# Kernel optimization log

Hardware: AMD Instinct MI355X
Metric: run time of the kernel (lower is better)

The kernel has to match this reference:

```python
import jax, jax.numpy as jnp
import numpy as np

VNUMS = [4248, 4258, 5327, 3721, 5404, 2818]
B, C, H, W = 12, 64, 192, 192
DV, HID, BOX = 128, 256, 32


def _roi_patches(imgs, pros, imgbatch, box_len=BOX):
    # torchvision roi_align (aligned=False, sampling_ratio -> 1 sample per 1x1 bin):
    # bilinear sample at bin centers x1 + (j+0.5), y1 + (i+0.5)
    ar = jnp.arange(box_len, dtype=pros.dtype) + 0.5
    xs = pros[:, 0:1] - box_len / 2.0 + ar  # [G, box]
    ys = pros[:, 1:2] - box_len / 2.0 + ar  # [G, box]
    img_g = imgs[imgbatch]  # [G, C, H, W]

    def sample_one(img_chw, ys1, xs1):
        yy, xx = jnp.meshgrid(ys1, xs1, indexing="ij")  # [box, box]
        def per_c(ch):
            return jax.scipy.ndimage.map_coordinates(ch, [yy, xx], order=1, mode="nearest")
        return jax.vmap(per_c)(img_chw)  # [C, box, box]

    return jax.vmap(sample_one)(img_g, ys, xs)  # [G, C, box, box]


def setup_inputs() -> dict:
    key = jax.random.key(0)
    ks = jax.random.split(key, 6)
    G = 2 * B
    gtypes = np.array([(g // 2) % 6 if g % 2 == 0 else ((g // 2) + 3) % 6 for g in range(G)], dtype=np.int64)
    vnums_g = np.array([VNUMS[t] for t in gtypes])
    off = np.concatenate([[0], np.cumsum(vnums_g)])
    Nv = int(off[-1])  # 103104
    gar_of_vert = np.repeat(np.arange(G), vnums_g)
    idxs = []
    for t in range(6):
        gl = np.nonzero(gtypes == t)[0]
        idxs.append(np.concatenate([off[g] + np.arange(VNUMS[t]) for g in gl]).astype(np.int32))
    Din = DV + C
    pros = jax.random.uniform(ks[1], (G, 2), jnp.float32) * (H - 2.0 * BOX) + BOX
    inp = {
        "imgs": jax.random.normal(ks[0], (B, C, H, W), jnp.float32),
        "pros": pros,
        "x_verts": jax.random.normal(ks[2], (Nv, DV), jnp.float32),
        "W1": jax.random.normal(ks[3], (6, Din, HID), jnp.float32) / np.sqrt(Din).astype(np.float32),
        "W2": jax.random.normal(ks[4], (6, HID, HID), jnp.float32) / np.sqrt(HID).astype(np.float32),
        "W3": jax.random.normal(ks[5], (6, HID, 3), jnp.float32) / np.sqrt(HID).astype(np.float32),
        "imgbatch": jnp.asarray(np.arange(G) // 2, jnp.int32),
        "gar_of_vert": jnp.asarray(gar_of_vert, jnp.int32),
    }
    for t in range(6):
        inp[f"idx_t{t}"] = jnp.asarray(idxs[t])
    return inp


def reference(imgs, pros, x_verts, W1, W2, W3, imgbatch, gar_of_vert,
              idx_t0, idx_t1, idx_t2, idx_t3, idx_t4, idx_t5):
    # 1) roi_align patch extraction + pooled per-garment image feature
    patches = _roi_patches(imgs, pros, imgbatch)        # [G, C, 32, 32]
    garf = patches.mean(axis=(2, 3))                     # [G, C]
    # 2) per-vertex feature = [vertex feat | garment image feat]
    feat = jnp.concatenate([x_verts, garf[gar_of_vert]], axis=-1)  # [Nv, DV+C]
    # 3) MoE-style dispatch per garment type -> per-type expert MLP -> scatter-combine
    out = jnp.zeros((x_verts.shape[0], 3), feat.dtype)
    for t, idx in enumerate([idx_t0, idx_t1, idx_t2, idx_t3, idx_t4, idx_t5]):
        ft = feat[idx]                                   # gather (dispatch)
        h = jax.nn.relu(ft @ W1[t])
        h = jax.nn.relu(h @ W2[t])
        out = out.at[idx].set(h @ W3[t])                 # scatter (combine)
    return out
```

## Files before the change

### kernel.cpp

```cpp
#include <hip/hip_runtime.h>

typedef __attribute__((ext_vector_type(8))) short short8;
typedef __attribute__((ext_vector_type(4))) float float4_;

__device__ __forceinline__ unsigned short f2bf(float f) {
    unsigned u = __float_as_uint(f);
    u += 0x7FFFu + ((u >> 16) & 1u);
    return (unsigned short)(u >> 16);
}

__global__ void garf_kernel(const float* __restrict__ imgs,
                            const float* __restrict__ pros,
                            const int* __restrict__ imgbatch,
                            float* __restrict__ garf) {
    __shared__ float part[4];
    const int tid = threadIdx.x;
    int g = blockIdx.x >> 6, c = blockIdx.x & 63;
    int b = imgbatch[g];
    float cx = pros[g * 2 + 0], cy = pros[g * 2 + 1];
    int i = tid >> 3;
    int j0 = (tid & 7) * 4;
    float y = cy - 16.0f + (float)i + 0.5f;
    float yf = floorf(y);
    float wy1 = y - yf, wy0 = 1.0f - wy1;
    int iy0 = min(max((int)yf, 0), 191), iy1 = min(max((int)yf + 1, 0), 191);
    const float* base = imgs + (size_t)(b * 64 + c) * 36864;
    const float* r0 = base + iy0 * 192;
    const float* r1 = base + iy1 * 192;
    float sum = 0.0f;
#pragma unroll
    for (int jj = 0; jj < 4; ++jj) {
        float x = cx - 16.0f + (float)(j0 + jj) + 0.5f;
        float xf = floorf(x);
        float wx1 = x - xf, wx0 = 1.0f - wx1;
        int ix0 = min(max((int)xf, 0), 191), ix1 = min(max((int)xf + 1, 0), 191);
        sum += wy0 * (wx0 * r0[ix0] + wx1 * r0[ix1]) +
               wy1 * (wx0 * r1[ix0] + wx1 * r1[ix1]);
    }
    for (int s = 32; s >= 1; s >>= 1) sum += __shfl_xor(sum, s);
    if ((tid & 63) == 0) part[tid >> 6] = sum;
    __syncthreads();
    if (tid == 0)
        garf[g * 64 + c] = (part[0] + part[1] + part[2] + part[3]) * (1.0f / 1024.0f);
}

struct MoEArgs {
    const float* x_verts;
    const int* gar;
    const int* idx[6];
    const float* W1;
    const float* W2;
    const float* W3;
    const float* garf;
    float* out;
    int cnt[6];
    int tile_end[6];
    int ntiles;
    int chunk;
};

__global__ __launch_bounds__(256, 1) void moe_kernel(MoEArgs a) {
    __shared__ __align__(16) char smem[65536 + 512];
    int* sidx = (int*)(smem + 65536);
    int* sg = sidx + 64;

    const int tid = threadIdx.x;
    const int lane = tid & 63, w = tid >> 6, q = lane >> 4, l = lane & 15;

    int start = blockIdx.x * a.chunk;
    int end = min(start + a.chunk, a.ntiles);

    short8 w1f[24], w2f[32], w3f[8];
    int tcur = -1;
    int p = 0;

    for (int tile = start; tile < end; ++tile, p ^= 1) {
        int t = 0;
        while (t < 5 && tile >= a.tile_end[t]) ++t;
        const int i0 = (tile - (t ? a.tile_end[t - 1] : 0)) * 64;
        const int cnt = a.cnt[t];
        const int* idx = a.idx[t];

        if (tid < 64) {
            int m = min(i0 + tid, cnt - 1);
            int vid = idx[m];
            sidx[tid] = vid;
            sg[tid] = a.gar[vid];
        }

        if (t != tcur) {
            tcur = t;
            const float* w1 = a.W1 + t * 49152;
            const float* w2 = a.W2 + t * 65536;
            const float* w3 = a.W3 + t * 768;
#pragma unroll
            for (int ks = 0; ks < 6; ++ks)
#pragma unroll
                for (int mt = 0; mt < 4; ++mt) {
                    const float* src = w1 + (ks * 32 + q * 8) * 256 + (w * 64 + mt * 16 + l);
                    short8 r;
#pragma unroll
                    for (int j = 0; j < 8; ++j) r[j] = (short)f2bf(src[j * 256]);
                    w1f[ks * 4 + mt] = r;
                }
#pragma unroll
            for (int ks = 0; ks < 8; ++ks)
#pragma unroll
                for (int mt = 0; mt < 4; ++mt) {
                    const float* src = w2 + (ks * 32 + q * 8) * 256 + (w * 64 + mt * 16 + l);
                    short8 r;
#pragma unroll
                    for (int j = 0; j < 8; ++j) r[j] = (short)f2bf(src[j * 256]);
                    w2f[ks * 4 + mt] = r;
                }
#pragma unroll
            for (int ks = 0; ks < 8; ++ks) {
                short8 r = {0, 0, 0, 0, 0, 0, 0, 0};
                if (l < 3) {
                    const float* src = w3 + (ks * 32 + q * 8) * 3 + l;
#pragma unroll
                    for (int j = 0; j < 8; ++j) r[j] = (short)f2bf(src[j * 3]);
                }
                w3f[ks] = r;
            }
        }
        __syncthreads();

        char* sF = smem + p * 32768;
        char* sH = smem + (p ^ 1) * 32768;

        for (int e = tid; e < 1536; e += 256) {
            int m = e / 24, u = e - (e / 24) * 24;
            const float* src;
            if (u < 16) src = a.x_verts + (size_t)sidx[m] * 128 + u * 8;
            else        src = a.garf + sg[m] * 64 + (u - 16) * 8;
            float4 v0 = ((const float4*)src)[0];
            float4 v1 = ((const float4*)src)[1];
            short8 pk;
            pk[0] = f2bf(v0.x); pk[1] = f2bf(v0.y); pk[2] = f2bf(v0.z); pk[3] = f2bf(v0.w);
            pk[4] = f2bf(v1.x); pk[5] = f2bf(v1.y); pk[6] = f2bf(v1.z); pk[7] = f2bf(v1.w);
            *(short8*)(sF + m * 384 + ((u ^ (m & 7)) * 16)) = pk;
        }
        const int v3 = w * 16 + l;
        const int myvid = sidx[v3];
        __syncthreads();

        float4_ acc[4][4] = {};
#pragma unroll
        for (int ks = 0; ks < 6; ++ks) {
            short8 bfr[4];
#pragma unroll
            for (int nt = 0; nt < 4; ++nt) {
                int v = nt * 16 + l;
                bfr[nt] = *(const short8*)(sF + v * 384 + (((ks * 4 + q) ^ (v & 7)) * 16));
            }
#pragma unroll
            for (int mt = 0; mt < 4; ++mt)
#pragma unroll
                for (int nt = 0; nt < 4; ++nt)
                    acc[mt][nt] = __builtin_amdgcn_mfma_f32_16x16x32_bf16(
                        w1f[ks * 4 + mt], bfr[nt], acc[mt][nt], 0, 0, 0);
        }
#pragma unroll
        for (int mt = 0; mt < 4; ++mt)
#pragma unroll
            for (int nt = 0; nt < 4; ++nt) {
                int v = nt * 16 + l;
                int hu8 = w * 16 + mt * 4 + q;
                int ku16 = hu8 >> 1, par = hu8 & 1;
                uint2 pk;
                pk.x = (unsigned)f2bf(fmaxf(acc[mt][nt][0], 0.0f)) |
                       ((unsigned)f2bf(fmaxf(acc[mt][nt][1], 0.0f)) << 16);
                pk.y = (unsigned)f2bf(fmaxf(acc[mt][nt][2], 0.0f)) |
                       ((unsigned)f2bf(fmaxf(acc[mt][nt][3], 0.0f)) << 16);
                *(uint2*)(sH + v * 512 + ((ku16 ^ (v & 7)) * 16) + par * 8) = pk;
            }
        __syncthreads();

#pragma unroll
        for (int mt = 0; mt < 4; ++mt)
#pragma unroll
            for (int nt = 0; nt < 4; ++nt) acc[mt][nt] = float4_{0.f, 0.f, 0.f, 0.f};
#pragma unroll
        for (int ks = 0; ks < 8; ++ks) {
            short8 bfr[4];
#pragma unroll
            for (int nt = 0; nt < 4; ++nt) {
                int v = nt * 16 + l;
                bfr[nt] = *(const short8*)(sH + v * 512 + (((ks * 4 + q) ^ (v & 7)) * 16));
            }
#pragma unroll
            for (int mt = 0; mt < 4; ++mt)
#pragma unroll
                for (int nt = 0; nt < 4; ++nt)
                    acc[mt][nt] = __builtin_amdgcn_mfma_f32_16x16x32_bf16(
                        w2f[ks * 4 + mt], bfr[nt], acc[mt][nt], 0, 0, 0);
        }
#pragma unroll
        for (int mt = 0; mt < 4; ++mt)
#pragma unroll
            for (int nt = 0; nt < 4; ++nt) {
                int v = nt * 16 + l;
                int hu8 = w * 16 + mt * 4 + q;
                int ku16 = hu8 >> 1, par = hu8 & 1;
                uint2 pk;
                pk.x = (unsigned)f2bf(fmaxf(acc[mt][nt][0], 0.0f)) |
                       ((unsigned)f2bf(fmaxf(acc[mt][nt][1], 0.0f)) << 16);
                pk.y = (unsigned)f2bf(fmaxf(acc[mt][nt][2], 0.0f)) |
                       ((unsigned)f2bf(fmaxf(acc[mt][nt][3], 0.0f)) << 16);
                *(uint2*)(sF + v * 512 + ((ku16 ^ (v & 7)) * 16) + par * 8) = pk;
            }
        __syncthreads();

        float4_ acc3 = {};
#pragma unroll
        for (int ks = 0; ks < 8; ++ks) {
            short8 b3 = *(const short8*)(sF + v3 * 512 + (((ks * 4 + q) ^ (v3 & 7)) * 16));
            acc3 = __builtin_amdgcn_mfma_f32_16x16x32_bf16(w3f[ks], b3, acc3, 0, 0, 0);
        }
        if (q == 0 && i0 + v3 < cnt) {
            float* o = a.out + (size_t)myvid * 3;
            o[0] = acc3[0]; o[1] = acc3[1]; o[2] = acc3[2];
        }
    }
}

extern "C" void kernel_launch(void* const* d_in, const int* in_sizes, int n_in,
                              void* d_out, int out_size, void* d_ws, size_t ws_size,
                              hipStream_t stream) {
    const float* imgs    = (const float*)d_in[0];
    const float* pros    = (const float*)d_in[1];
    const float* x_verts = (const float*)d_in[2];
    const float* W1      = (const float*)d_in[3];
    const float* W2      = (const float*)d_in[4];
    const float* W3      = (const float*)d_in[5];
    const int* imgbatch  = (const int*)d_in[6];
    const int* gar       = (const int*)d_in[7];

    float* garf = (float*)d_ws;

    garf_kernel<<<24 * 64, 256, 0, stream>>>(imgs, pros, imgbatch, garf);

    MoEArgs a;
    a.x_verts = x_verts;
    a.gar = gar;
    for (int t = 0; t < 6; ++t) a.idx[t] = (const int*)d_in[8 + t];
    a.W1 = W1; a.W2 = W2; a.W3 = W3;
    a.garf = garf;
    a.out = (float*)d_out;
    int tiles = 0;
    for (int t = 0; t < 6; ++t) {
        a.cnt[t] = in_sizes[8 + t];
        tiles += (a.cnt[t] + 63) / 64;
        a.tile_end[t] = tiles;
    }
    a.ntiles = tiles;
    a.chunk = (tiles + 255) / 256;
    moe_kernel<<<256, 256, 0, stream>>>(a);
}
```

Baseline: 291.6 us.

## Split MoE tile work across 8 waves and balance tiles per block

Doubles the MoE block to 512 threads. Each wave now holds half as many weight fragments (2 M-tiles instead of 4), and the final 3-wide layer is split over K halves with a shared-memory reduction. Tiles are spread evenly across blocks with a proportional start/end instead of a ceil chunk. All vertex indices for the block are prefetched once up front, and the feature gather issues all of its loads before converting. The aim is to cut per-wave register pressure, raise latency hiding and even out load imbalance, at the cost of an extra barrier and reduction per tile. The 448-entry index buffer assumes at most 7 tiles per block.

```diff
diff --git a/kernel.cpp b/kernel.cpp
--- a/kernel.cpp
+++ b/kernel.cpp
@@ -44,6 +44,7 @@
         garf[g * 64 + c] = (part[0] + part[1] + part[2] + part[3]) * (1.0f / 1024.0f);
 }
 
+#define NBLK 256
 struct MoEArgs {
     const float* x_verts;
     const int* gar;
@@ -56,37 +57,47 @@
     int cnt[6];
     int tile_end[6];
     int ntiles;
-    int chunk;
 };
 
-__global__ __launch_bounds__(256, 1) void moe_kernel(MoEArgs a) {
-    __shared__ __align__(16) char smem[65536 + 512];
-    int* sidx = (int*)(smem + 65536);
-    int* sg = sidx + 64;
+__global__ __launch_bounds__(512, 2) void moe_kernel(MoEArgs a) {
+    __shared__ __align__(16) char smem[65536];
+    __shared__ int sidx_all[448], sg_all[448];
+    __shared__ float pb[2 * 64 * 4];
 
     const int tid = threadIdx.x;
     const int lane = tid & 63, w = tid >> 6, q = lane >> 4, l = lane & 15;
 
-    int start = blockIdx.x * a.chunk;
-    int end = min(start + a.chunk, a.ntiles);
-
-    short8 w1f[24], w2f[32], w3f[8];
+    const int start = (blockIdx.x * a.ntiles) / NBLK;
+    const int end = ((int)(blockIdx.x + 1) * a.ntiles) / NBLK;
+    const int nt_blk = end - start;
+
+    if (tid < nt_blk * 64) {
+        int s = tid >> 6, lm = tid & 63;
+        int tile = start + s;
+        int t = 0;
+        while (t < 5 && tile >= a.tile_end[t]) ++t;
+        int i0 = (tile - (t ? a.tile_end[t - 1] : 0)) * 64;
+        int m = min(i0 + lm, a.cnt[t] - 1);
+        int vid = a.idx[t][m];
+        sidx_all[tid] = vid;
+        sg_all[tid] = a.gar[vid];
+    }
+
+    short8 w1f[12], w2f[16], w3f[4];
+    const int kh = w >> 2;
+    const int vs = w & 3;
     int tcur = -1;
     int p = 0;
-
-    for (int tile = start; tile < end; ++tile, p ^= 1) {
+    __syncthreads();
+
+    for (int s = 0; s < nt_blk; ++s, p ^= 1) {
+        const int tile = start + s;
         int t = 0;
         while (t < 5 && tile >= a.tile_end[t]) ++t;
         const int i0 = (tile - (t ? a.tile_end[t - 1] : 0)) * 64;
         const int cnt = a.cnt[t];
-        const int* idx = a.idx[t];
-
-        if (tid < 64) {
-            int m = min(i0 + tid, cnt - 1);
-            int vid = idx[m];
-            sidx[tid] = vid;
-            sg[tid] = a.gar[vid];
-        }
+        const int* sidx = sidx_all + s * 64;
+        const int* sg = sg_all + s * 64;
 
         if (t != tcur) {
             tcur = t;
@@ -96,56 +107,66 @@
 #pragma unroll
             for (int ks = 0; ks < 6; ++ks)
 #pragma unroll
-                for (int mt = 0; mt < 4; ++mt) {
-                    const float* src = w1 + (ks * 32 + q * 8) * 256 + (w * 64 + mt * 16 + l);
+                for (int mt = 0; mt < 2; ++mt) {
+                    const float* src = w1 + (ks * 32 + q * 8) * 256 + (w * 32 + mt * 16 + l);
                     short8 r;
 #pragma unroll
                     for (int j = 0; j < 8; ++j) r[j] = (short)f2bf(src[j * 256]);
-                    w1f[ks * 4 + mt] = r;
+                    w1f[ks * 2 + mt] = r;
                 }
 #pragma unroll
             for (int ks = 0; ks < 8; ++ks)
 #pragma unroll
-                for (int mt = 0; mt < 4; ++mt) {
-                    const float* src = w2 + (ks * 32 + q * 8) * 256 + (w * 64 + mt * 16 + l);
+                for (int mt = 0; mt < 2; ++mt) {
+                    const float* src = w2 + (ks * 32 + q * 8) * 256 + (w * 32 + mt * 16 + l);
                     short8 r;
 #pragma unroll
                     for (int j = 0; j < 8; ++j) r[j] = (short)f2bf(src[j * 256]);
-                    w2f[ks * 4 + mt] = r;
+                    w2f[ks * 2 + mt] = r;
                 }
 #pragma unroll
-            for (int ks = 0; ks < 8; ++ks) {
+            for (int i = 0; i < 4; ++i) {
+                int ks = kh * 4 + i;
                 short8 r = {0, 0, 0, 0, 0, 0, 0, 0};
                 if (l < 3) {
                     const float* src = w3 + (ks * 32 + q * 8) * 3 + l;
 #pragma unroll
                     for (int j = 0; j < 8; ++j) r[j] = (short)f2bf(src[j * 3]);
                 }
-                w3f[ks] = r;
-            }
-        }
-        __syncthreads();
+                w3f[i] = r;
+            }
+        }
 
         char* sF = smem + p * 32768;
         char* sH = smem + (p ^ 1) * 32768;
 
-        for (int e = tid; e < 1536; e += 256) {
-            int m = e / 24, u = e - (e / 24) * 24;
-            const float* src;
-            if (u < 16) src = a.x_verts + (size_t)sidx[m] * 128 + u * 8;
-            else        src = a.garf + sg[m] * 64 + (u - 16) * 8;
-            float4 v0 = ((const float4*)src)[0];
-            float4 v1 = ((const float4*)src)[1];
-            short8 pk;
-            pk[0] = f2bf(v0.x); pk[1] = f2bf(v0.y); pk[2] = f2bf(v0.z); pk[3] = f2bf(v0.w);
-            pk[4] = f2bf(v1.x); pk[5] = f2bf(v1.y); pk[6] = f2bf(v1.z); pk[7] = f2bf(v1.w);
-            *(short8*)(sF + m * 384 + ((u ^ (m & 7)) * 16)) = pk;
-        }
-        const int v3 = w * 16 + l;
-        const int myvid = sidx[v3];
-        __syncthreads();
-
-        float4_ acc[4][4] = {};
+        {
+            float4 va[3][2];
+            int mm[3], uu[3];
+#pragma unroll
+            for (int i = 0; i < 3; ++i) {
+                int e = tid + i * 512;
+                int m = e / 24, u = e - m * 24;
+                mm[i] = m; uu[i] = u;
+                const float* src;
+                if (u < 16) src = a.x_verts + (size_t)sidx[m] * 128 + u * 8;
+                else        src = a.garf + sg[m] * 64 + (u - 16) * 8;
+                va[i][0] = ((const float4*)src)[0];
+                va[i][1] = ((const float4*)src)[1];
+            }
+#pragma unroll
+            for (int i = 0; i < 3; ++i) {
+                short8 pk;
+                pk[0] = f2bf(va[i][0].x); pk[1] = f2bf(va[i][0].y);
+                pk[2] = f2bf(va[i][0].z); pk[3] = f2bf(va[i][0].w);
+                pk[4] = f2bf(va[i][1].x); pk[5] = f2bf(va[i][1].y);
+                pk[6] = f2bf(va[i][1].z); pk[7] = f2bf(va[i][1].w);
+                *(short8*)(sF + mm[i] * 384 + ((uu[i] ^ (mm[i] & 7)) * 16)) = pk;
+            }
+        }
+        __syncthreads();
+
+        float4_ acc[2][4] = {};
 #pragma unroll
         for (int ks = 0; ks < 6; ++ks) {
             short8 bfr[4];
@@ -155,18 +176,18 @@
                 bfr[nt] = *(const short8*)(sF + v * 384 + (((ks * 4 + q) ^ (v & 7)) * 16));
             }
 #pragma unroll
-            for (int mt = 0; mt < 4; ++mt)
+            for (int mt = 0; mt < 2; ++mt)
 #pragma unroll
                 for (int nt = 0; nt < 4; ++nt)
                     acc[mt][nt] = __builtin_amdgcn_mfma_f32_16x16x32_bf16(
-                        w1f[ks * 4 + mt], bfr[nt], acc[mt][nt], 0, 0, 0);
-        }
-#pragma unroll
-        for (int mt = 0; mt < 4; ++mt)
-#pragma unroll
-            for (int nt = 0; nt < 4; ++nt) {
-                int v = nt * 16 + l;
-                int hu8 = w * 16 + mt * 4 + q;
+                        w1f[ks * 2 + mt], bfr[nt], acc[mt][nt], 0, 0, 0);
+        }
+#pragma unroll
+        for (int mt = 0; mt < 2; ++mt)
+#pragma unroll
+            for (int nt = 0; nt < 4; ++nt) {
+                int v = nt * 16 + l;
+                int hu8 = w * 8 + mt * 4 + q;
                 int ku16 = hu8 >> 1, par = hu8 & 1;
                 uint2 pk;
                 pk.x = (unsigned)f2bf(fmaxf(acc[mt][nt][0], 0.0f)) |
@@ -178,7 +199,7 @@
         __syncthreads();
 
 #pragma unroll
-        for (int mt = 0; mt < 4; ++mt)
+        for (int mt = 0; mt < 2; ++mt)
 #pragma unroll
             for (int nt = 0; nt < 4; ++nt) acc[mt][nt] = float4_{0.f, 0.f, 0.f, 0.f};
 #pragma unroll
@@ -190,18 +211,18 @@
                 bfr[nt] = *(const short8*)(sH + v * 512 + (((ks * 4 + q) ^ (v & 7)) * 16));
             }
 #pragma unroll
-            for (int mt = 0; mt < 4; ++mt)
+            for (int mt = 0; mt < 2; ++mt)
 #pragma unroll
                 for (int nt = 0; nt < 4; ++nt)
                     acc[mt][nt] = __builtin_amdgcn_mfma_f32_16x16x32_bf16(
-                        w2f[ks * 4 + mt], bfr[nt], acc[mt][nt], 0, 0, 0);
-        }
-#pragma unroll
-        for (int mt = 0; mt < 4; ++mt)
-#pragma unroll
-            for (int nt = 0; nt < 4; ++nt) {
-                int v = nt * 16 + l;
-                int hu8 = w * 16 + mt * 4 + q;
+                        w2f[ks * 2 + mt], bfr[nt], acc[mt][nt], 0, 0, 0);
+        }
+#pragma unroll
+        for (int mt = 0; mt < 2; ++mt)
+#pragma unroll
+            for (int nt = 0; nt < 4; ++nt) {
+                int v = nt * 16 + l;
+                int hu8 = w * 8 + mt * 4 + q;
                 int ku16 = hu8 >> 1, par = hu8 & 1;
                 uint2 pk;
                 pk.x = (unsigned)f2bf(fmaxf(acc[mt][nt][0], 0.0f)) |
@@ -213,14 +234,25 @@
         __syncthreads();
 
         float4_ acc3 = {};
-#pragma unroll
-        for (int ks = 0; ks < 8; ++ks) {
+        const int v3 = vs * 16 + l;
+#pragma unroll
+        for (int i = 0; i < 4; ++i) {
+            int ks = kh * 4 + i;
             short8 b3 = *(const short8*)(sF + v3 * 512 + (((ks * 4 + q) ^ (v3 & 7)) * 16));
-            acc3 = __builtin_amdgcn_mfma_f32_16x16x32_bf16(w3f[ks], b3, acc3, 0, 0, 0);
-        }
-        if (q == 0 && i0 + v3 < cnt) {
-            float* o = a.out + (size_t)myvid * 3;
-            o[0] = acc3[0]; o[1] = acc3[1]; o[2] = acc3[2];
+            acc3 = __builtin_amdgcn_mfma_f32_16x16x32_bf16(w3f[i], b3, acc3, 0, 0, 0);
+        }
+        if (q == 0) {
+            float* d = pb + kh * 256 + v3 * 4;
+            d[0] = acc3[0]; d[1] = acc3[1]; d[2] = acc3[2];
+        }
+        __syncthreads();
+
+        if (tid < 192) {
+            int v = tid / 3, j = tid - v * 3;
+            if (i0 + v < cnt) {
+                float sum = pb[v * 4 + j] + pb[256 + v * 4 + j];
+                a.out[(size_t)sidx[v] * 3 + j] = sum;
+            }
         }
     }
 }
@@ -255,6 +287,5 @@
         a.tile_end[t] = tiles;
     }
     a.ntiles = tiles;
-    a.chunk = (tiles + 255) / 256;
-    moe_kernel<<<256, 256, 0, stream>>>(a);
-}
+    moe_kernel<<<NBLK, 512, 0, stream>>>(a);
+}
```

After: 288.5 us. Within noise of the previous version (-1.0%).
